# Kernel optimization log

Measured on AMD Instinct MI355X. Metric: run time of the kernel, lower is better.

Reference implementation:

```python
import jax, jax.numpy as jnp
import numpy as np

N = 50000          # nodes
F = 128            # feature dim (indim = outdim)
AVG_DEG = 12       # random edges per node (plus one self-loop)
AVG_D_LOG = 2.6    # avg_d['log'] used by PNA scalers
EPS = 1e-5         # PNA std epsilon / BatchNorm eps


def setup_inputs() -> dict:
    key = jax.random.key(0)
    k1, k2, k3, k4 = jax.random.split(key, 4)
    h = jax.random.normal(k1, (N, F), dtype=jnp.float32)
    E_rand = N * AVG_DEG
    src_r = jax.random.randint(k2, (E_rand,), 0, N)
    dst_r = jax.random.randint(k3, (E_rand,), 0, N)
    loop = jnp.arange(N)
    src = jnp.concatenate([src_r, loop]).astype(jnp.int64) if jax.config.jax_enable_x64 else jnp.concatenate([src_r, loop]).astype(jnp.int32)
    dst = jnp.concatenate([dst_r, loop]).astype(src.dtype)
    concat_dim = F * (1 + 4 * 3)  # indim * (1 + n_aggr * n_scalers)
    W = jax.random.normal(k4, (concat_dim, F), dtype=jnp.float32) * (1.0 / np.sqrt(concat_dim))
    b = jnp.zeros((F,), dtype=jnp.float32)
    gamma = jnp.ones((F,), dtype=jnp.float32)
    beta = jnp.zeros((F,), dtype=jnp.float32)
    return {"h": h, "src": src, "dst": dst, "W": W, "b": b, "gamma": gamma, "beta": beta}


def _pna_forward(h, W, b, gamma, beta, src, dst):
    n = h.shape[0]
    m = h[src]                                            # [E, F] gathered mailbox
    deg = jax.ops.segment_sum(jnp.ones(src.shape[0], h.dtype), dst, num_segments=n)
    deg = jnp.maximum(deg, 1.0)[:, None]                  # every node has a self-loop
    s = jax.ops.segment_sum(m, dst, num_segments=n)
    mean = s / deg
    mx = jax.ops.segment_max(m, dst, num_segments=n)
    mn = jax.ops.segment_min(m, dst, num_segments=n)
    mean_sq = jax.ops.segment_sum(m * m, dst, num_segments=n) / deg
    std = jnp.sqrt(jax.nn.relu(mean_sq - mean * mean) + EPS)
    agg = jnp.concatenate([mean, mx, mn, std], axis=1)    # [N, 4F]
    logd = jnp.log(deg + 1.0)                             # [N, 1]
    scaled = jnp.concatenate([agg,
                              agg * (logd / AVG_D_LOG),
                              agg * (AVG_D_LOG / logd)], axis=1)  # [N, 12F]
    hc = jnp.concatenate([h, scaled], axis=1)             # [N, 13F]
    out = hc @ W + b                                      # posttrans (single linear)
    out = jax.nn.relu(out)                                # activation (dropout p=0)
    mu = out.mean(axis=0)                                 # BatchNorm1d, training stats
    var = out.var(axis=0)                                 # biased variance (torch)
    out = gamma * (out - mu) * jax.lax.rsqrt(var + EPS) + beta
    return out


def reference(h, src, dst, W, b, gamma, beta):
    return _pna_forward(h, W, b, gamma, beta, src, dst)
```

## Files before the change

kernel.cpp:

```cpp
#include <hip/hip_runtime.h>
#include <math.h>

#define FDIM 128
#define AVG_D_LOGF 2.6f
#define BN_EPS 1e-5f
#define NK 10

using f32x4 = __attribute__((ext_vector_type(4))) float;
using s16x8 = __attribute__((ext_vector_type(8))) short;
using u16x8 = __attribute__((ext_vector_type(8))) unsigned short;

__device__ __forceinline__ unsigned short f2bf(float x) {
  unsigned int u = __float_as_uint(x);
  u += 0x7FFFu + ((u >> 16) & 1u);
  return (unsigned short)(u >> 16);
}
__device__ __forceinline__ float bf2f(unsigned short u) {
  return __uint_as_float(((unsigned int)u) << 16);
}

__device__ __forceinline__ void gload16(const void* g, void* l) {
  __builtin_amdgcn_global_load_lds(
      (const __attribute__((address_space(1))) void*)g,
      (__attribute__((address_space(3))) void*)l, 16, 0, 0);
}

__global__ void conv_h(const float* __restrict__ h, unsigned short* __restrict__ hb, int total8) {
  int i = blockIdx.x * 256 + threadIdx.x;
  if (i >= total8) return;
  const f32x4* sp = (const f32x4*)h + (size_t)i * 2;
  f32x4 v0 = sp[0], v1 = sp[1];
  u16x8 o;
  o[0] = f2bf(v0[0]); o[1] = f2bf(v0[1]); o[2] = f2bf(v0[2]); o[3] = f2bf(v0[3]);
  o[4] = f2bf(v1[0]); o[5] = f2bf(v1[1]); o[6] = f2bf(v1[2]); o[7] = f2bf(v1[3]);
  *((u16x8*)hb + i) = o;
}

__global__ void deg_kernel(const int* __restrict__ dst, int* __restrict__ deg, int E) {
  int i = blockIdx.x * 256 + threadIdx.x;
  if (i < E) atomicAdd(&deg[dst[i]], 1);
}

__global__ void scan1(const int* __restrict__ deg, int* __restrict__ offs,
                      int* __restrict__ bsums, int n) {
  __shared__ int tmp[256];
  int t = threadIdx.x, i = blockIdx.x * 256 + t;
  int v = (i < n) ? deg[i] : 0;
  tmp[t] = v; __syncthreads();
  for (int d = 1; d < 256; d <<= 1) {
    int x = (t >= d) ? tmp[t - d] : 0;
    __syncthreads();
    tmp[t] += x;
    __syncthreads();
  }
  if (i < n) offs[i] = tmp[t] - v;
  if (t == 255) bsums[blockIdx.x] = tmp[255];
}

__global__ void scan2(int* __restrict__ bsums, int nb) {
  __shared__ int tmp[256];
  int t = threadIdx.x;
  int v = (t < nb) ? bsums[t] : 0;
  tmp[t] = v; __syncthreads();
  for (int d = 1; d < 256; d <<= 1) {
    int x = (t >= d) ? tmp[t - d] : 0;
    __syncthreads();
    tmp[t] += x;
    __syncthreads();
  }
  if (t < nb) bsums[t] = tmp[t] - v;
}

__global__ void scan3(int* __restrict__ offs, const int* __restrict__ bsums, int n, int E) {
  int i = blockIdx.x * 256 + threadIdx.x;
  if (i < n) offs[i] += bsums[blockIdx.x];
  if (i == 0) offs[n] = E;
}

__global__ void csr_fill(const int* __restrict__ src, const int* __restrict__ dst,
                         const int* __restrict__ offs, int* __restrict__ cursor,
                         int* __restrict__ csr, int E) {
  int i = blockIdx.x * 256 + threadIdx.x;
  if (i < E) {
    int d = dst[i];
    int pos = offs[d] + atomicAdd(&cursor[d], 1);
    csr[pos] = src[i];
  }
}

__global__ __launch_bounds__(256) void agg_kernel(
    const unsigned short* __restrict__ hb, const int* __restrict__ csr,
    const int* __restrict__ offs, unsigned short* __restrict__ aggb,
    float2* __restrict__ s12a, int n) {
  const int gw = (blockIdx.x * 256 + threadIdx.x) >> 6;
  const int lane = threadIdx.x & 63;
  if (gw >= n) return;
  const int beg = offs[gw], end = offs[gw + 1];
  const unsigned int* hp = (const unsigned int*)hb;
  float s0 = 0.f, s1 = 0.f, q0 = 0.f, q1 = 0.f;
  float mx0 = -INFINITY, mx1 = -INFINITY, mn0 = INFINITY, mn1 = INFINITY;
  int e = beg;
  for (; e + 4 <= end; e += 4) {
    int i0 = csr[e], i1 = csr[e + 1], i2 = csr[e + 2], i3 = csr[e + 3];
    unsigned int a = hp[(size_t)i0 * 64 + lane];
    unsigned int b = hp[(size_t)i1 * 64 + lane];
    unsigned int c = hp[(size_t)i2 * 64 + lane];
    unsigned int d = hp[(size_t)i3 * 64 + lane];
    float a0 = bf2f((unsigned short)a), a1 = bf2f((unsigned short)(a >> 16));
    float b0 = bf2f((unsigned short)b), b1 = bf2f((unsigned short)(b >> 16));
    float c0 = bf2f((unsigned short)c), c1 = bf2f((unsigned short)(c >> 16));
    float d0 = bf2f((unsigned short)d), d1 = bf2f((unsigned short)(d >> 16));
    s0 += (a0 + b0) + (c0 + d0); s1 += (a1 + b1) + (c1 + d1);
    q0 += (a0 * a0 + b0 * b0) + (c0 * c0 + d0 * d0);
    q1 += (a1 * a1 + b1 * b1) + (c1 * c1 + d1 * d1);
    mx0 = fmaxf(fmaxf(mx0, a0), fmaxf(b0, fmaxf(c0, d0)));
    mx1 = fmaxf(fmaxf(mx1, a1), fmaxf(b1, fmaxf(c1, d1)));
    mn0 = fminf(fminf(mn0, a0), fminf(b0, fminf(c0, d0)));
    mn1 = fminf(fminf(mn1, a1), fminf(b1, fminf(c1, d1)));
  }
  for (; e < end; ++e) {
    int i0 = csr[e];
    unsigned int a = hp[(size_t)i0 * 64 + lane];
    float a0 = bf2f((unsigned short)a), a1 = bf2f((unsigned short)(a >> 16));
    s0 += a0; s1 += a1;
    q0 += a0 * a0; q1 += a1 * a1;
    mx0 = fmaxf(mx0, a0); mx1 = fmaxf(mx1, a1);
    mn0 = fminf(mn0, a0); mn1 = fminf(mn1, a1);
  }
  float degf = (float)(end - beg);
  if (degf < 1.f) degf = 1.f;
  const float inv = 1.f / degf;
  float me0 = s0 * inv, me1 = s1 * inv;
  float v0 = q0 * inv - me0 * me0, v1 = q1 * inv - me1 * me1;
  float st0 = sqrtf(fmaxf(v0, 0.f) + BN_EPS);
  float st1 = sqrtf(fmaxf(v1, 0.f) + BN_EPS);
  unsigned int base = (unsigned int)gw * 512u + (unsigned int)lane * 2u;
  *(unsigned int*)&aggb[base      ] = (unsigned int)f2bf(me0) | ((unsigned int)f2bf(me1) << 16);
  *(unsigned int*)&aggb[base + 128] = (unsigned int)f2bf(mx0) | ((unsigned int)f2bf(mx1) << 16);
  *(unsigned int*)&aggb[base + 256] = (unsigned int)f2bf(mn0) | ((unsigned int)f2bf(mn1) << 16);
  *(unsigned int*)&aggb[base + 384] = (unsigned int)f2bf(st0) | ((unsigned int)f2bf(st1) << 16);
  if (lane == 0) {
    float logd = logf(degf + 1.f);
    s12a[gw] = make_float2(logd / AVG_D_LOGF, AVG_D_LOGF / logd);
  }
}

__global__ void conv_wt(const float* __restrict__ W, unsigned short* __restrict__ wBT, int K) {
  int idx = blockIdx.x * 256 + threadIdx.x;
  if (idx < K * FDIM) {
    int k = idx >> 7, j = idx & 127;
    wBT[(size_t)j * K + k] = f2bf(W[idx]);
  }
}

__global__ __launch_bounds__(256, 2) void gemm_kernel(
    const unsigned short* __restrict__ hb, const unsigned short* __restrict__ wBT,
    const unsigned short* __restrict__ aggb, const float2* __restrict__ s12a,
    const float* __restrict__ bias, float* __restrict__ out,
    float* __restrict__ bnsum, float* __restrict__ bnsq, int n, int K) {
  __shared__ s16x8 AsB[2][1024];
  __shared__ s16x8 BsB[2][3][512];
  const int t = threadIdx.x;
  const int lane = t & 63;
  const int w = t >> 6;
  const int wr = w >> 1, wc = w & 1;
  const int hi = lane >> 4, lr = lane & 15, rx7 = lr & 7;
  const int bx = blockIdx.x;
  const int m0 = (bx >> 1) * 128;
  const int n0 = (bx & 1) * 64;

  f32x4 acc[3][4][2] = {};

  auto stage = [&](int ss, int buf) {
    const bool ph1 = (ss < 2);
    #pragma unroll
    for (int i = 0; i < 4; ++i) {
      int unit = w * 256 + i * 64 + lane;
      int row = unit >> 3, x = unit & 7;
      int node = m0 + row; if (node >= n) node = n - 1;
      int xo = (x ^ (row & 7)) << 3;
      const unsigned short* src = ph1
          ? hb   + (size_t)node * FDIM + ss * 64 + xo
          : aggb + (size_t)node * 512 + (ss - 2) * 64 + xo;
      gload16(src, &AsB[buf][w * 256 + i * 64]);
    }
    const int nsec = ph1 ? 1 : 3;
    for (int s = 0; s < nsec; ++s) {
      int koff = ph1 ? ss * 64 : (FDIM + s * 512 + (ss - 2) * 64);
      #pragma unroll
      for (int i = 0; i < 2; ++i) {
        int unit = w * 128 + i * 64 + lane;
        int row = unit >> 3, x = unit & 7;
        const unsigned short* src =
            wBT + (size_t)(n0 + row) * K + koff + ((x ^ (row & 7)) << 3);
        gload16(src, &BsB[buf][s][w * 128 + i * 64]);
      }
    }
  };

  stage(0, 0);
  int cur = 0;
  for (int step = 0; step < NK; ++step) {
    if (step + 1 < NK) {
      stage(step + 1, cur ^ 1);
      if (step + 1 < 2) asm volatile("s_waitcnt vmcnt(6)" ::: "memory");
      else              asm volatile("s_waitcnt vmcnt(10)" ::: "memory");
    } else {
      asm volatile("s_waitcnt vmcnt(0)" ::: "memory");
    }
    asm volatile("s_barrier" ::: "memory");
    #pragma unroll
    for (int ks = 0; ks < 2; ++ks) {
      s16x8 a[4];
      #pragma unroll
      for (int m = 0; m < 4; ++m) {
        int row = wr * 64 + m * 16 + lr;
        a[m] = AsB[cur][row * 8 + ((ks * 4 + hi) ^ rx7)];
      }
      #pragma unroll
      for (int s = 0; s < 3; ++s) {
        if (step < 2 && s > 0) continue;
        int rb = wc * 32 + lr;
        s16x8 b0 = BsB[cur][s][rb * 8 + ((ks * 4 + hi) ^ rx7)];
        s16x8 b1 = BsB[cur][s][(rb + 16) * 8 + ((ks * 4 + hi) ^ rx7)];
        #pragma unroll
        for (int m = 0; m < 4; ++m) {
          acc[s][m][0] = __builtin_amdgcn_mfma_f32_16x16x32_bf16(a[m], b0, acc[s][m][0], 0, 0, 0);
          acc[s][m][1] = __builtin_amdgcn_mfma_f32_16x16x32_bf16(a[m], b1, acc[s][m][1], 0, 0, 0);
        }
      }
    }
    asm volatile("s_barrier" ::: "memory");
    cur ^= 1;
  }

  float* red = (float*)&AsB[0][0];
  if (t < 128) red[t] = 0.f;
  __syncthreads();

  const float bv0 = bias[n0 + wc * 32 + lr];
  const float bv1 = bias[n0 + wc * 32 + 16 + lr];
  float cs[2] = {0.f, 0.f}, cq[2] = {0.f, 0.f};
  #pragma unroll
  for (int m = 0; m < 4; ++m) {
    #pragma unroll
    for (int i = 0; i < 4; ++i) {
      int grow = m0 + wr * 64 + m * 16 + hi * 4 + i;
      if (grow >= n) continue;
      float2 sv = s12a[grow];
      #pragma unroll
      for (int nn = 0; nn < 2; ++nn) {
        float v = acc[0][m][nn][i] + sv.x * acc[1][m][nn][i] + sv.y * acc[2][m][nn][i]
                + (nn ? bv1 : bv0);
        v = fmaxf(v, 0.f);
        out[(size_t)grow * FDIM + n0 + wc * 32 + nn * 16 + lr] = v;
        cs[nn] += v; cq[nn] += v * v;
      }
    }
  }
  #pragma unroll
  for (int nn = 0; nn < 2; ++nn) {
    int lc = wc * 32 + nn * 16 + lr;
    atomicAdd(&red[lc], cs[nn]);
    atomicAdd(&red[64 + lc], cq[nn]);
  }
  __syncthreads();
  if (t < 64)       atomicAdd(&bnsum[n0 + t], red[t]);
  else if (t < 128) atomicAdd(&bnsq[n0 + t - 64], red[t]);
}

__global__ void bn_norm(float* __restrict__ out, const float* __restrict__ bnsum,
                        const float* __restrict__ bnsq, const float* __restrict__ gamma,
                        const float* __restrict__ beta, int n) {
  const int j = threadIdx.x & 127;
  const float invN = 1.f / (float)n;
  const float mu = bnsum[j] * invN;
  const float var = bnsq[j] * invN - mu * mu;
  const float rs = rsqrtf(var + BN_EPS);
  const float sc = gamma[j] * rs;
  const float sh = beta[j] - mu * sc;
  const int gt = blockIdx.x * 256 + threadIdx.x;
  const int row0 = gt >> 7;
  const int rstride = (gridDim.x * 256) >> 7;
  for (int i = row0; i < n; i += rstride) {
    size_t idx = (size_t)i * FDIM + j;
    out[idx] = out[idx] * sc + sh;
  }
}

extern "C" void kernel_launch(void* const* d_in, const int* in_sizes, int n_in,
                              void* d_out, int out_size, void* d_ws, size_t ws_size,
                              hipStream_t stream) {
  const float* h     = (const float*)d_in[0];
  const int*   src   = (const int*)d_in[1];
  const int*   dst   = (const int*)d_in[2];
  const float* W     = (const float*)d_in[3];
  const float* bias  = (const float*)d_in[4];
  const float* gamma = (const float*)d_in[5];
  const float* beta  = (const float*)d_in[6];
  float* out = (float*)d_out;

  const int n = in_sizes[0] / FDIM;
  const int E = in_sizes[1];
  const int K = in_sizes[3] / FDIM;

  char* base = (char*)d_ws;
  size_t off = 0;
  auto alloc = [&](size_t bytes) -> void* {
    void* p = base + off;
    off += (bytes + 255) & ~(size_t)255;
    return p;
  };
  int*   deg    = (int*)  alloc(4ull * n);
  int*   cursor = (int*)  alloc(4ull * n);
  float* bnsum  = (float*)alloc(512);
  float* bnsq   = (float*)alloc(512);
  const size_t zlen = off;
  int*    offs  = (int*)  alloc(4ull * (n + 1));
  int*    bsums = (int*)  alloc(4ull * 256);
  int*    csr   = (int*)  alloc(4ull * E);
  float2* s12a  = (float2*)alloc(8ull * n);
  unsigned short* aggb = (unsigned short*)alloc(2ull * (size_t)n * 512);
  unsigned short* wBT  = (unsigned short*)alloc(2ull * (size_t)K * FDIM);
  unsigned short* hb   = (unsigned short*)alloc(2ull * (size_t)n * FDIM);
  (void)ws_size; (void)n_in; (void)out_size;

  const int eb = (E + 255) / 256;
  const int nb = (n + 255) / 256;

  hipMemsetAsync(d_ws, 0, zlen, stream);
  conv_h<<<(n * FDIM / 8 + 255) / 256, 256, 0, stream>>>(h, hb, n * FDIM / 8);
  conv_wt<<<(K * FDIM + 255) / 256, 256, 0, stream>>>(W, wBT, K);
  deg_kernel<<<eb, 256, 0, stream>>>(dst, deg, E);
  scan1<<<nb, 256, 0, stream>>>(deg, offs, bsums, n);
  scan2<<<1, 256, 0, stream>>>(bsums, nb);
  scan3<<<nb, 256, 0, stream>>>(offs, bsums, n, E);
  csr_fill<<<eb, 256, 0, stream>>>(src, dst, offs, cursor, csr, E);
  agg_kernel<<<(n + 3) / 4, 256, 0, stream>>>(hb, csr, offs, aggb, s12a, n);
  const int gblocks = ((n + 127) / 128) * 2;
  gemm_kernel<<<gblocks, 256, 0, stream>>>(hb, wBT, aggb, s12a, bias,
                                           out, bnsum, bnsq, n, K);
  bn_norm<<<1024, 256, 0, stream>>>(out, bnsum, bnsq, gamma, beta, n);
}
```

Baseline: 179.6 us.

## Fuse prep kernels, single-buffer GEMM LDS for more occupancy, remap blocks per XCD

Merges the h conversion, W transpose-conversion and degree-count kernels into one launch, removing two kernel launches. The GEMM drops its LDS double buffer in favour of a simple load-sync-compute loop and raises launch bounds from 2 to 3 blocks per CU. It also remaps block indices so consecutive tiles land on the same XCD for L2 locality. The trade is that load/compute overlap inside each block now depends on other resident blocks rather than on prefetching.

Measured after the change: 175.9 us. 2.1% less time.

```diff
diff --git a/kernel.cpp b/kernel.cpp
--- a/kernel.cpp
+++ b/kernel.cpp
@@ -25,20 +25,25 @@
       (__attribute__((address_space(3))) void*)l, 16, 0, 0);
 }
 
-__global__ void conv_h(const float* __restrict__ h, unsigned short* __restrict__ hb, int total8) {
+__global__ void prep_kernel(const float* __restrict__ h, unsigned short* __restrict__ hb,
+                            const float* __restrict__ W, unsigned short* __restrict__ wBT,
+                            const int* __restrict__ dst, int* __restrict__ deg,
+                            int w0, int w1, int w2, int K) {
   int i = blockIdx.x * 256 + threadIdx.x;
-  if (i >= total8) return;
-  const f32x4* sp = (const f32x4*)h + (size_t)i * 2;
-  f32x4 v0 = sp[0], v1 = sp[1];
-  u16x8 o;
-  o[0] = f2bf(v0[0]); o[1] = f2bf(v0[1]); o[2] = f2bf(v0[2]); o[3] = f2bf(v0[3]);
-  o[4] = f2bf(v1[0]); o[5] = f2bf(v1[1]); o[6] = f2bf(v1[2]); o[7] = f2bf(v1[3]);
-  *((u16x8*)hb + i) = o;
-}
-
-__global__ void deg_kernel(const int* __restrict__ dst, int* __restrict__ deg, int E) {
-  int i = blockIdx.x * 256 + threadIdx.x;
-  if (i < E) atomicAdd(&deg[dst[i]], 1);
+  if (i < w0) {
+    const f32x4* sp = (const f32x4*)h + (size_t)i * 2;
+    f32x4 v0 = sp[0], v1 = sp[1];
+    u16x8 o;
+    o[0] = f2bf(v0[0]); o[1] = f2bf(v0[1]); o[2] = f2bf(v0[2]); o[3] = f2bf(v0[3]);
+    o[4] = f2bf(v1[0]); o[5] = f2bf(v1[1]); o[6] = f2bf(v1[2]); o[7] = f2bf(v1[3]);
+    *((u16x8*)hb + i) = o;
+  } else if (i < w0 + w1) {
+    int idx = i - w0;
+    int k = idx >> 7, j = idx & 127;
+    wBT[(size_t)j * K + k] = f2bf(W[idx]);
+  } else if (i < w0 + w1 + w2) {
+    atomicAdd(&deg[dst[i - w0 - w1]], 1);
+  }
 }
 
 __global__ void scan1(const int* __restrict__ deg, int* __restrict__ offs,
@@ -145,33 +150,30 @@
   }
 }
 
-__global__ void conv_wt(const float* __restrict__ W, unsigned short* __restrict__ wBT, int K) {
-  int idx = blockIdx.x * 256 + threadIdx.x;
-  if (idx < K * FDIM) {
-    int k = idx >> 7, j = idx & 127;
-    wBT[(size_t)j * K + k] = f2bf(W[idx]);
-  }
-}
-
-__global__ __launch_bounds__(256, 2) void gemm_kernel(
+__global__ __launch_bounds__(256, 3) void gemm_kernel(
     const unsigned short* __restrict__ hb, const unsigned short* __restrict__ wBT,
     const unsigned short* __restrict__ aggb, const float2* __restrict__ s12a,
     const float* __restrict__ bias, float* __restrict__ out,
     float* __restrict__ bnsum, float* __restrict__ bnsq, int n, int K) {
-  __shared__ s16x8 AsB[2][1024];
-  __shared__ s16x8 BsB[2][3][512];
+  __shared__ s16x8 As[1024];
+  __shared__ s16x8 Bs[3][512];
   const int t = threadIdx.x;
   const int lane = t & 63;
   const int w = t >> 6;
   const int wr = w >> 1, wc = w & 1;
   const int hi = lane >> 4, lr = lane & 15, rx7 = lr & 7;
-  const int bx = blockIdx.x;
+
+  const int nwg = gridDim.x;
+  const int q = nwg >> 3, r = nwg & 7;
+  const int xcd = blockIdx.x & 7, jj = blockIdx.x >> 3;
+  const int bx = (xcd < r ? xcd * (q + 1) : r * (q + 1) + (xcd - r) * q) + jj;
+
   const int m0 = (bx >> 1) * 128;
   const int n0 = (bx & 1) * 64;
 
   f32x4 acc[3][4][2] = {};
 
-  auto stage = [&](int ss, int buf) {
+  auto stage = [&](int ss) {
     const bool ph1 = (ss < 2);
     #pragma unroll
     for (int i = 0; i < 4; ++i) {
@@ -182,7 +184,7 @@
       const unsigned short* src = ph1
           ? hb   + (size_t)node * FDIM + ss * 64 + xo
           : aggb + (size_t)node * 512 + (ss - 2) * 64 + xo;
-      gload16(src, &AsB[buf][w * 256 + i * 64]);
+      gload16(src, &As[w * 256 + i * 64]);
     }
     const int nsec = ph1 ? 1 : 3;
     for (int s = 0; s < nsec; ++s) {
@@ -193,36 +195,28 @@
         int row = unit >> 3, x = unit & 7;
         const unsigned short* src =
             wBT + (size_t)(n0 + row) * K + koff + ((x ^ (row & 7)) << 3);
-        gload16(src, &BsB[buf][s][w * 128 + i * 64]);
+        gload16(src, &Bs[s][w * 128 + i * 64]);
       }
     }
   };
 
-  stage(0, 0);
-  int cur = 0;
   for (int step = 0; step < NK; ++step) {
-    if (step + 1 < NK) {
-      stage(step + 1, cur ^ 1);
-      if (step + 1 < 2) asm volatile("s_waitcnt vmcnt(6)" ::: "memory");
-      else              asm volatile("s_waitcnt vmcnt(10)" ::: "memory");
-    } else {
-      asm volatile("s_waitcnt vmcnt(0)" ::: "memory");
-    }
-    asm volatile("s_barrier" ::: "memory");
+    stage(step);
+    __syncthreads();
     #pragma unroll
     for (int ks = 0; ks < 2; ++ks) {
       s16x8 a[4];
       #pragma unroll
       for (int m = 0; m < 4; ++m) {
         int row = wr * 64 + m * 16 + lr;
-        a[m] = AsB[cur][row * 8 + ((ks * 4 + hi) ^ rx7)];
+        a[m] = As[row * 8 + ((ks * 4 + hi) ^ rx7)];
       }
       #pragma unroll
       for (int s = 0; s < 3; ++s) {
         if (step < 2 && s > 0) continue;
         int rb = wc * 32 + lr;
-        s16x8 b0 = BsB[cur][s][rb * 8 + ((ks * 4 + hi) ^ rx7)];
-        s16x8 b1 = BsB[cur][s][(rb + 16) * 8 + ((ks * 4 + hi) ^ rx7)];
+        s16x8 b0 = Bs[s][rb * 8 + ((ks * 4 + hi) ^ rx7)];
+        s16x8 b1 = Bs[s][(rb + 16) * 8 + ((ks * 4 + hi) ^ rx7)];
         #pragma unroll
         for (int m = 0; m < 4; ++m) {
           acc[s][m][0] = __builtin_amdgcn_mfma_f32_16x16x32_bf16(a[m], b0, acc[s][m][0], 0, 0, 0);
@@ -230,11 +224,10 @@
         }
       }
     }
-    asm volatile("s_barrier" ::: "memory");
-    cur ^= 1;
-  }
-
-  float* red = (float*)&AsB[0][0];
+    __syncthreads();
+  }
+
+  float* red = (float*)&As[0];
   if (t < 128) red[t] = 0.f;
   __syncthreads();
 
@@ -327,11 +320,13 @@
 
   const int eb = (E + 255) / 256;
   const int nb = (n + 255) / 256;
+  const int w0 = n * FDIM / 8;
+  const int w1 = K * FDIM;
+  const int w2 = E;
 
   hipMemsetAsync(d_ws, 0, zlen, stream);
-  conv_h<<<(n * FDIM / 8 + 255) / 256, 256, 0, stream>>>(h, hb, n * FDIM / 8);
-  conv_wt<<<(K * FDIM + 255) / 256, 256, 0, stream>>>(W, wBT, K);
-  deg_kernel<<<eb, 256, 0, stream>>>(dst, deg, E);
+  prep_kernel<<<(w0 + w1 + w2 + 255) / 256, 256, 0, stream>>>(h, hb, W, wBT, dst, deg,
+                                                              w0, w1, w2, K);
   scan1<<<nb, 256, 0, stream>>>(deg, offs, bsums, n);
   scan2<<<1, 256, 0, stream>>>(bsums, nb);
   scan3<<<nb, 256, 0, stream>>>(offs, bsums, n, E);
```
